# Kernel tuning notes

Hardware: AMD Instinct MI355X
Metric: run time of the kernel (lower is better)

The kernel has to match this reference:

```python
import jax, jax.numpy as jnp
import numpy as np

EPS_STAB = 1e-9   # numerical_stabilizer default
BN_EPS = 1e-5     # flax BatchNorm default epsilon


def setup_inputs() -> dict:
    key = jax.random.key(0)
    ks = jax.random.split(key, 5)
    B, N, C = 2, 4096, 512
    s = 1.0 / np.sqrt(C)
    d = {"inputs": jax.random.normal(ks[0], (B, N, C), jnp.float32)}
    # 1x1 convs == pointwise linear maps [C_in, C_out] + bias
    for i, w in enumerate(["Wq", "Wk", "Wv", "Wo"]):
        d[w] = jax.random.normal(ks[1 + i], (C, C), jnp.float32) * s
    for b in ["bq", "bk", "bv", "bo"]:
        d[b] = jnp.zeros((C,), jnp.float32)
    # BatchNorm (inference: use_running_average=True since train=False)
    d["bn_scale"] = jnp.ones((C,), jnp.float32)
    d["bn_bias"] = jnp.zeros((C,), jnp.float32)
    d["bn_mean"] = jnp.zeros((C,), jnp.float32)
    d["bn_var"] = jnp.ones((C,), jnp.float32)
    return d


def reference(inputs, Wq, bq, Wk, bk, Wv, bv, Wo, bo,
              bn_scale, bn_bias, bn_mean, bn_var):
    # QKV via 1x1 conv == dense projection. [B, N, C]
    q = inputs @ Wq + bq
    k = inputs @ Wk + bk
    v = inputs @ Wv + bv
    # scores [B, M, N]; softmax over last axis (N)
    att = jax.nn.softmax(jnp.einsum('bmc,bnc->bmn', q, k), axis=-1)
    # non-standard renorm: divide by column sums (axis=1 == M axis)
    att = att / (EPS_STAB + jnp.sum(att, axis=1, keepdims=True))
    # faithful to einsum '...MN,...NC->...NC': sum attention over M, scale v
    out = v * jnp.sum(att, axis=1)[..., None]
    # output 1x1 conv
    out = out @ Wo + bo
    # BatchNorm with running stats (feature axis -1)
    out = (out - bn_mean) * jax.lax.rsqrt(bn_var + BN_EPS) * bn_scale + bn_bias
    return jax.nn.relu(out) + inputs
```

## Files before the change

### kernel.cpp

```cpp
#include <hip/hip_runtime.h>
#include <hip/hip_bf16.h>

typedef unsigned short u16;
typedef unsigned int u32;
typedef __attribute__((ext_vector_type(8))) short short8;
typedef __attribute__((ext_vector_type(4))) float f32x4;
typedef __attribute__((ext_vector_type(4))) unsigned int u32x4;

__device__ __forceinline__ u16 f2bf(float f) {
    union { float f; unsigned u; } v; v.f = f;
    unsigned r = v.u + 0x7fffu + ((v.u >> 16) & 1u);
    return (u16)(r >> 16);
}

__device__ __forceinline__ float fexp2(float x) {
#if __has_builtin(__builtin_amdgcn_exp2f)
    return __builtin_amdgcn_exp2f(x);
#else
    return __expf(x * 0.6931471805599453f);
#endif
}

template <int CTRL>
__device__ __forceinline__ float fdpp(float x) {
    int xi = __builtin_bit_cast(int, x);
    int r = __builtin_amdgcn_update_dpp(0, xi, CTRL, 0xF, 0xF, true);
    return __builtin_bit_cast(float, r);
}
__device__ __forceinline__ float dpp_max16(float m) {
    m = fmaxf(m, fdpp<0xB1>(m));
    m = fmaxf(m, fdpp<0x4E>(m));
    m = fmaxf(m, fdpp<0x141>(m));
    m = fmaxf(m, fdpp<0x140>(m));
    return m;
}
__device__ __forceinline__ float dpp_sum16(float s) {
    s += fdpp<0xB1>(s);
    s += fdpp<0x4E>(s);
    s += fdpp<0x141>(s);
    s += fdpp<0x140>(s);
    return s;
}

#if __has_builtin(__builtin_amdgcn_cvt_pk_fp8_f32) && \
    __has_builtin(__builtin_amdgcn_cvt_f32_fp8)
#define FP8_HW 1
#else
#define FP8_HW 0
#endif

#if !FP8_HW
__device__ __forceinline__ u32 sw_fp8(float x) {
    union { float f; u32 u; } v; v.f = x;
    int E = (int)(v.u >> 23) - 127;
    if (x < 0.001953125f) return 0;
    if (E < -6) return (u32)(x * 512.0f + 0.5f);
    u32 m = v.u & 0x7fffffu;
    u32 r = (m + 0x80000u) >> 20;
    u32 bits = ((u32)(E + 7) << 3) + r;
    return bits > 0x7eu ? 0x7eu : bits;
}
__device__ __forceinline__ float sw_fp8d(u32 b) {
    u32 e = (b >> 3) & 15u, m = b & 7u;
    if (e == 0) return (float)m * 0.001953125f;
    union { u32 u; float f; } v; v.u = ((e + 120u) << 23) | (m << 20);
    return v.f;
}
#endif

__device__ __forceinline__ u32 fp8x4_pack(float p0, float p1, float p2, float p3) {
#if FP8_HW
    u32 v = (u32)__builtin_amdgcn_cvt_pk_fp8_f32(p0, p1, 0, false);
    v = (u32)__builtin_amdgcn_cvt_pk_fp8_f32(p2, p3, (int)v, true);
    return v;
#else
    return sw_fp8(p0) | (sw_fp8(p1) << 8) | (sw_fp8(p2) << 16) | (sw_fp8(p3) << 24);
#endif
}

#if FP8_HW
#define FP8_DEC(v, s) __builtin_amdgcn_cvt_f32_fp8((int)(v), (s))
#else
#define FP8_DEC(v, s) sw_fp8d(((v) >> ((s) * 8)) & 0xffu)
#endif

__device__ __forceinline__ void async_cp16(const u16* g, u16* l) {
    __builtin_amdgcn_global_load_lds(
        (const __attribute__((address_space(1))) void*)g,
        (__attribute__((address_space(3))) void*)l, 16, 0, 0);
}

__device__ __forceinline__ short8 mfma_ld(const u16* base, int off) {
    return *(const short8*)&base[off];
}

__device__ __forceinline__ void stage_half_A(const u16* __restrict__ Q,
                                             u16* dst, int kn, int half,
                                             int wid, int srow, int scol) {
#pragma unroll
    for (int c = 0; c < 2; c++) {
        int win = (wid >> 2) * 16 + half * 8 + (wid & 3) * 2 + c;
        async_cp16(Q + (size_t)(win * 8 + srow) * 512 + kn + scol,
                   dst + win * 512);
    }
}
__device__ __forceinline__ void stage_half_B(const u16* __restrict__ K,
                                             u16* dst, int kn, int half,
                                             int wid, int srow, int scol) {
#pragma unroll
    for (int c = 0; c < 2; c++) {
        int win = (wid >> 1) * 8 + half * 4 + (wid & 1) * 2 + c;
        async_cp16(K + (size_t)(win * 8 + srow) * 512 + kn + scol,
                   dst + win * 512);
    }
}

__device__ __forceinline__ void core256(const u16* __restrict__ A,
                                        const u16* __restrict__ B,
                                        u16* As0, u16* As1,
                                        u16* Bs0, u16* Bs1,
                                        f32x4 acc[8][4], int tid) {
    int lane = tid & 63, wid = tid >> 6;
    int quad = lane >> 4, l15 = lane & 15;
    int wm = wid >> 2, wn = wid & 3;
    int Gw = lane ^ ((lane >> 3) & 7);
    int srow = Gw >> 3, scol = (Gw & 7) * 8;
    int rl = l15 & 7, winl = l15 >> 3;
    int Pr[2];
#pragma unroll
    for (int h = 0; h < 2; h++)
        Pr[h] = (rl * 8 + ((quad + h * 4) ^ rl)) * 8;

    stage_half_A(A, As0, 0, 0, wid, srow, scol);
    stage_half_B(B, Bs0, 0, 0, wid, srow, scol);
    stage_half_B(B, Bs0, 0, 1, wid, srow, scol);
    stage_half_A(A, As0, 0, 1, wid, srow, scol);
    asm volatile("s_waitcnt vmcnt(0)" ::: "memory");
    __builtin_amdgcn_s_barrier();
    asm volatile("" ::: "memory");

    for (int kt = 0; kt < 8; ++kt) {
        const u16* Ac = (kt & 1) ? As1 : As0;
        const u16* Bc = (kt & 1) ? Bs1 : Bs0;
        u16* An = (kt & 1) ? As0 : As1;
        u16* Bn = (kt & 1) ? Bs0 : Bs1;
        int kn = (kt + 1) * 64;
        bool pf = (kt < 7);
        short8 af[4][2], bf0[2][2], bf1[2][2];
#pragma unroll
        for (int ph = 0; ph < 4; ++ph) {
            const int ih = ph >> 1;
            const int jh = (ph ^ (ph >> 1)) & 1;
            if (ph == 0) {
#pragma unroll
                for (int h = 0; h < 2; h++)
#pragma unroll
                    for (int ii = 0; ii < 4; ii++)
                        af[ii][h] = mfma_ld(
                            Ac, (wm * 16 + ii * 2 + winl) * 512 + Pr[h]);
#pragma unroll
                for (int h = 0; h < 2; h++)
#pragma unroll
                    for (int jj = 0; jj < 2; jj++)
                        bf0[jj][h] = mfma_ld(
                            Bc, (wn * 8 + jj * 2 + winl) * 512 + Pr[h]);
            } else if (ph == 1) {
#pragma unroll
                for (int h = 0; h < 2; h++)
#pragma unroll
                    for (int jj = 0; jj < 2; jj++)
                        bf1[jj][h] = mfma_ld(
                            Bc, (wn * 8 + 4 + jj * 2 + winl) * 512 + Pr[h]);
            } else if (ph == 2) {
#pragma unroll
                for (int h = 0; h < 2; h++)
#pragma unroll
                    for (int ii = 0; ii < 4; ii++)
                        af[ii][h] = mfma_ld(
                            Ac, (wm * 16 + 8 + ii * 2 + winl) * 512 + Pr[h]);
            }
            if (pf) {
                if (ph == 0) {
                    stage_half_A(A, An, kn, 0, wid, srow, scol);
                    stage_half_B(B, Bn, kn, 0, wid, srow, scol);
                } else if (ph == 1) {
                    stage_half_B(B, Bn, kn, 1, wid, srow, scol);
                } else if (ph == 2) {
                    stage_half_A(A, An, kn, 1, wid, srow, scol);
                }
            }
            if (ph == 1) {
                if (pf) asm volatile("s_waitcnt vmcnt(6)" ::: "memory");
                else    asm volatile("s_waitcnt vmcnt(0)" ::: "memory");
            }
            if (ph == 3) asm volatile("s_waitcnt vmcnt(2)" ::: "memory");
            asm volatile("" ::: "memory");
            __builtin_amdgcn_s_barrier();
            asm volatile("s_waitcnt lgkmcnt(0)" ::: "memory");
            __builtin_amdgcn_s_setprio(1);
            if (jh == 0) {
#pragma unroll
                for (int h = 0; h < 2; h++)
#pragma unroll
                    for (int ii = 0; ii < 4; ii++)
#pragma unroll
                        for (int jj = 0; jj < 2; jj++)
                            acc[ih * 4 + ii][jj] =
                                __builtin_amdgcn_mfma_f32_16x16x32_bf16(
                                    af[ii][h], bf0[jj][h],
                                    acc[ih * 4 + ii][jj], 0, 0, 0);
            } else {
#pragma unroll
                for (int h = 0; h < 2; h++)
#pragma unroll
                    for (int ii = 0; ii < 4; ii++)
#pragma unroll
                        for (int jj = 0; jj < 2; jj++)
                            acc[ih * 4 + ii][2 + jj] =
                                __builtin_amdgcn_mfma_f32_16x16x32_bf16(
                                    af[ii][h], bf1[jj][h],
                                    acc[ih * 4 + ii][2 + jj], 0, 0, 0);
            }
            __builtin_amdgcn_s_setprio(0);
            asm volatile("" ::: "memory");
            __builtin_amdgcn_s_barrier();
            asm volatile("" ::: "memory");
        }
    }
}

__device__ __forceinline__ void gemm512_r64(const u16* __restrict__ A,
                                            const u16* __restrict__ B,
                                            u16* As, u16* Bs,
                                            f32x4 acc[2][4], int tid) {
    const int lane = tid & 63, w = tid >> 6;
    const int quad = lane >> 4, l15 = lane & 15;
    const int wm = tid >> 7, wn = (tid >> 6) & 1;
    const int Gw = lane ^ ((lane >> 3) & 7);
    const int srow = Gw >> 3;
    const int scol = (Gw & 7) * 8;
    const int rl = l15 & 7;
    const int winl = l15 >> 3;
    int Pr[2];
#pragma unroll
    for (int h = 0; h < 2; h++)
        Pr[h] = (rl * 8 + ((quad + h * 4) ^ rl)) * 8;
    const int winA0 = (wm * 32) >> 3, winB0 = (wn * 64) >> 3;
    for (int k0 = 0; k0 < 512; k0 += 64) {
        __syncthreads();
#pragma unroll
        for (int t = 0; t < 2; t++) {
            int win = w * 2 + t;
            async_cp16(A + (size_t)(win * 8 + srow) * 512 + k0 + scol,
                       As + win * 512);
        }
#pragma unroll
        for (int t = 0; t < 4; t++) {
            int win = w * 4 + t;
            async_cp16(B + (size_t)(win * 8 + srow) * 512 + k0 + scol,
                       Bs + win * 512);
        }
        __syncthreads();
#pragma unroll
        for (int h = 0; h < 2; h++) {
            short8 af[2], bfr[4];
#pragma unroll
            for (int i = 0; i < 2; i++)
                af[i] = mfma_ld(As, (winA0 + i * 2 + winl) * 512 + Pr[h]);
#pragma unroll
            for (int j = 0; j < 4; j++)
                bfr[j] = mfma_ld(Bs, (winB0 + j * 2 + winl) * 512 + Pr[h]);
#pragma unroll
            for (int i = 0; i < 2; i++)
#pragma unroll
                for (int j = 0; j < 4; j++)
                    acc[i][j] = __builtin_amdgcn_mfma_f32_16x16x32_bf16(
                        af[i], bfr[j], acc[i][j], 0, 0, 0);
        }
    }
}

__global__ void prep(const float* __restrict__ X, const float* __restrict__ W0,
                     const float* __restrict__ W1, const float* __restrict__ W2,
                     const float* __restrict__ W3, u16* __restrict__ Xb,
                     u16* __restrict__ T0, u16* __restrict__ T1,
                     u16* __restrict__ T2, u16* __restrict__ T3,
                     float* __restrict__ Sg) {
    __shared__ float tile[32][33];
    int id = blockIdx.x, tid = threadIdx.x;
    if (id == 5120) {
        float4 z = {0.f, 0.f, 0.f, 0.f};
#pragma unroll
        for (int t = 0; t < 8; t++) ((float4*)Sg)[tid + t * 256] = z;
        return;
    }
    if (id < 4096) {
        int idx = (id * 256 + tid) * 4;
        float4 v = *(const float4*)&X[idx];
        ushort4 o;
        o.x = f2bf(v.x); o.y = f2bf(v.y); o.z = f2bf(v.z); o.w = f2bf(v.w);
        *(ushort4*)&Xb[idx] = o;
        return;
    }
    int t = id - 4096;
    int z = t >> 8, rem = t & 255;
    int bo_ = (rem & 15) * 32, bi = (rem >> 4) * 32;
    const float* src; u16* dst;
    switch (z) {
        case 0: src = W0; dst = T0; break;
        case 1: src = W1; dst = T1; break;
        case 2: src = W2; dst = T2; break;
        default: src = W3; dst = T3; break;
    }
    int tx = tid & 31, ty = tid >> 5;
#pragma unroll
    for (int s = 0; s < 4; s++) {
        int i = bi + ty + s * 8;
        tile[ty + s * 8][tx] = src[i * 512 + bo_ + tx];
    }
    __syncthreads();
#pragma unroll
    for (int s = 0; s < 4; s++) {
        int o = bo_ + ty + s * 8;
        dst[o * 512 + bi + tx] = f2bf(tile[tx][ty + s * 8]);
    }
}

__global__ __launch_bounds__(512, 2) void gemm_qkv(
    const u16* __restrict__ Xb, const u16* __restrict__ Wall,
    const float* __restrict__ bq, const float* __restrict__ bk,
    const float* __restrict__ bv, u16* __restrict__ Qall) {
    __shared__ __align__(16) u16 As[2][16384];
    __shared__ __align__(16) u16 Bs[2][16384];
    int tid = threadIdx.x;
    int m0 = blockIdx.x * 256, n0 = blockIdx.y * 256, z = blockIdx.z;
    const u16* A = Xb + (size_t)m0 * 512;
    const u16* B = Wall + (size_t)z * 262144 + (size_t)n0 * 512;
    f32x4 acc[8][4];
#pragma unroll
    for (int i = 0; i < 8; i++)
#pragma unroll
        for (int j = 0; j < 4; j++) acc[i][j] = (f32x4){0.f, 0.f, 0.f, 0.f};
    core256(A, B, &As[0][0], &As[1][0], &Bs[0][0], &Bs[1][0], acc, tid);

    const float* bias = (z == 0) ? bq : (z == 1) ? bk : bv;
    const float qs = (z == 0) ? 1.44269504088896340736f : 1.0f;
    u16* C = Qall + (size_t)z * 4194304;
    int lane = tid & 63, wid = tid >> 6;
    int quad = lane >> 4, l15 = lane & 15;
    int wm = wid >> 2, wn = wid & 3;
#pragma unroll
    for (int j = 0; j < 4; j++) {
        int n = n0 + wn * 64 + j * 16 + l15;
        float bvv = bias[n];
#pragma unroll
        for (int i = 0; i < 8; i++)
#pragma unroll
            for (int rg = 0; rg < 4; rg++) {
                int m = m0 + wm * 128 + i * 16 + quad * 4 + rg;
                C[(size_t)m * 512 + n] = f2bf((acc[i][j][rg] + bvv) * qs);
            }
    }
}

__global__ __launch_bounds__(512, 2) void attn_pass1p(
    const u16* __restrict__ Qb, const u16* __restrict__ Kb,
    float2* __restrict__ statsP, u32* __restrict__ Pbuf) {
    __shared__ __align__(16) u16 As[2][16384];
    __shared__ __align__(16) u16 Bs[2][16384];
    int tid = threadIdx.x;
    int mblk = blockIdx.x, nblk = blockIdx.y, b = blockIdx.z;
    const u16* Q = Qb + ((size_t)(b * 4096 + mblk * 256)) * 512;
    const u16* K = Kb + ((size_t)(b * 4096 + nblk * 256)) * 512;
    int lane = tid & 63, wid = tid >> 6;
    int quad = lane >> 4, l15 = lane & 15;
    int wm = wid >> 2, wn = wid & 3;

    f32x4 acc[8][4];
#pragma unroll
    for (int i = 0; i < 8; i++)
#pragma unroll
        for (int j = 0; j < 4; j++) acc[i][j] = (f32x4){0.f, 0.f, 0.f, 0.f};
    core256(Q, K, &As[0][0], &As[1][0], &Bs[0][0], &Bs[1][0], acc, tid);

    u32* Pt = Pbuf + ((size_t)((b * 16 + mblk) * 16 + nblk)) * 16384;
    int ch = nblk * 4 + wn;
    float2* Sp = statsP + ((size_t)(b * 64 + ch)) * 4096;
    int mbase = mblk * 256 + wm * 128;
#pragma unroll
    for (int i = 0; i < 8; i++) {
        u32x4 pk;
#pragma unroll
        for (int rg = 0; rg < 4; rg++) {
            float v0 = acc[i][0][rg], v1 = acc[i][1][rg];
            float v2 = acc[i][2][rg], v3 = acc[i][3][rg];
            float Mt = fmaxf(fmaxf(v0, v1), fmaxf(v2, v3));
            Mt = dpp_max16(Mt);
            float e8 = Mt - 8.0f;
            float p0 = fexp2(v0 - e8), p1 = fexp2(v1 - e8);
            float p2 = fexp2(v2 - e8), p3 = fexp2(v3 - e8);
            pk[rg] = fp8x4_pack(p0, p1, p2, p3);
            float L = dpp_sum16(p0 + p1 + p2 + p3);
            if (l15 == 0)
                Sp[mbase + i * 16 + quad * 4 + rg] =
                    make_float2(Mt, L * 0.00390625f);
        }
        *(u32x4*)&Pt[i * 2048 + tid * 4] = pk;
    }
}

__global__ void reduce_stats2(const float2* __restrict__ statsP,
                              float* __restrict__ cstat) {
    int t = blockIdx.x * 256 + threadIdx.x;
    int b = t >> 12, m = t & 4095;
    const float2* sp = statsP + (size_t)b * 64 * 4096 + m;
    float M = -INFINITY;
#pragma unroll 4
    for (int ch = 0; ch < 64; ch++) M = fmaxf(M, sp[(size_t)ch * 4096].x);
    float Z = 0.f;
#pragma unroll 4
    for (int ch = 0; ch < 64; ch++) {
        float2 p = sp[(size_t)ch * 4096];
        Z += p.y * fexp2(p.x - M);
    }
    cstat[t] = M + __log2f(Z);
}

__global__ __launch_bounds__(512) void colsum(
    const u32* __restrict__ Pbuf, const float2* __restrict__ statsP,
    const float* __restrict__ cstat, float* __restrict__ Sg) {
    int tid = threadIdx.x, lane = tid & 63, wid = tid >> 6;
    int quad = lane >> 4, l15 = lane & 15;
    int wm = wid >> 2, wn = wid & 3;
    int nblk = blockIdx.x, mgrp = blockIdx.y, b = blockIdx.z;
    int ch = nblk * 4 + wn;
    const float2* Sp = statsP + ((size_t)(b * 64 + ch)) * 4096;
    const float* Cp = cstat + (size_t)b * 4096;
    float cp[4] = {0.f, 0.f, 0.f, 0.f};
    for (int mb = 0; mb < 2; mb++) {
        int mblk = mgrp * 2 + mb;
        const u32* Pt =
            Pbuf + ((size_t)((b * 16 + mblk) * 16 + nblk)) * 16384;
#pragma unroll
        for (int i = 0; i < 8; i++) {
            int r0 = mblk * 256 + wm * 128 + i * 16 + quad * 4;
            float4 s01 = *(const float4*)&Sp[r0];
            float4 s23 = *(const float4*)&Sp[r0 + 2];
            float4 cv = *(const float4*)&Cp[r0];
            float fv[4] = {fexp2(s01.x - 8.0f - cv.x),
                           fexp2(s01.z - 8.0f - cv.y),
                           fexp2(s23.x - 8.0f - cv.z),
                           fexp2(s23.z - 8.0f - cv.w)};
            float fm = fmaxf(fmaxf(fv[0], fv[1]), fmaxf(fv[2], fv[3]));
            if (fm > 3.469446951953614e-18f) {
                u32x4 e4 = *(const u32x4*)&Pt[i * 2048 + tid * 4];
#pragma unroll
                for (int rg = 0; rg < 4; rg++) {
                    u32 e = e4[rg];
                    cp[0] += FP8_DEC(e, 0) * fv[rg];
                    cp[1] += FP8_DEC(e, 1) * fv[rg];
                    cp[2] += FP8_DEC(e, 2) * fv[rg];
                    cp[3] += FP8_DEC(e, 3) * fv[rg];
                }
            }
        }
    }
#pragma unroll
    for (int j = 0; j < 4; j++) {
        float s = cp[j];
        s += __shfl_xor(s, 16);
        s += __shfl_xor(s, 32);
        if (lane < 16)
            atomicAdd(&Sg[b * 4096 + nblk * 256 + wn * 64 + j * 16 + l15], s);
    }
}

__global__ __launch_bounds__(256) void gemm_final(
    const u16* __restrict__ A, const u16* __restrict__ Bt,
    const float* __restrict__ Sg, const float* __restrict__ bo,
    const float* __restrict__ g, const float* __restrict__ bb,
    const float* __restrict__ mean, const float* __restrict__ var,
    const float* __restrict__ X, float* __restrict__ out) {
    __shared__ __align__(16) u16 As[4096];
    __shared__ __align__(16) u16 Bs[8192];
    int tid = threadIdx.x;
    int m0 = blockIdx.x * 64, n0 = blockIdx.y * 128;
    f32x4 acc[2][4];
#pragma unroll
    for (int i = 0; i < 2; i++)
#pragma unroll
        for (int j = 0; j < 4; j++) acc[i][j] = (f32x4){0.f, 0.f, 0.f, 0.f};
    gemm512_r64(A + (size_t)m0 * 512, Bt + (size_t)n0 * 512, As, Bs, acc, tid);
    int lane = tid & 63, quad = lane >> 4, l15 = lane & 15;
    int wm = tid >> 7, wn = (tid >> 6) & 1;
    float sc[2][4];
#pragma unroll
    for (int i = 0; i < 2; i++) {
        float4 s = *(const float4*)&Sg[m0 + wm * 32 + i * 16 + quad * 4];
        float v[4] = {s.x, s.y, s.z, s.w};
#pragma unroll
        for (int rg = 0; rg < 4; rg++) sc[i][rg] = v[rg] / (1e-9f + v[rg]);
    }
#pragma unroll
    for (int j = 0; j < 4; j++) {
        int n = n0 + wn * 64 + j * 16 + l15;
        float aj = rsqrtf(var[n] + 1e-5f) * g[n];
        float cj = bb[n] - mean[n] * aj;
        float bj = bo[n];
#pragma unroll
        for (int i = 0; i < 2; i++)
#pragma unroll
            for (int rg = 0; rg < 4; rg++) {
                int m = m0 + wm * 32 + i * 16 + quad * 4 + rg;
                float x = acc[i][j][rg] * sc[i][rg] + bj;
                float y = x * aj + cj;
                out[(size_t)m * 512 + n] = fmaxf(y, 0.f) + X[(size_t)m * 512 + n];
            }
    }
}

extern "C" void kernel_launch(void* const* d_in, const int* in_sizes, int n_in,
                              void* d_out, int out_size, void* d_ws, size_t ws_size,
                              hipStream_t stream) {
    const float* X  = (const float*)d_in[0];
    const float* Wq = (const float*)d_in[1];
    const float* Wk = (const float*)d_in[2];
    const float* Wv = (const float*)d_in[3];
    const float* Wo = (const float*)d_in[4];
    const float* bq = (const float*)d_in[5];
    const float* bk = (const float*)d_in[6];
    const float* bv = (const float*)d_in[7];
    const float* bo = (const float*)d_in[8];
    const float* g    = (const float*)d_in[9];
    const float* bb   = (const float*)d_in[10];
    const float* mean = (const float*)d_in[11];
    const float* var  = (const float*)d_in[12];
    float* out = (float*)d_out;

    char* ws = (char*)d_ws;
    u16* Xb  = (u16*)(ws + 0);
    u16* Wqt = (u16*)(ws + 8388608);
    u16* Wot = (u16*)(ws + 9961472);
    u16* Qb  = (u16*)(ws + 10485760);
    u16* Kb  = (u16*)(ws + 18874368);
    u16* Vb  = (u16*)(ws + 27262976);
    float2* statsP = (float2*)(ws + 35651584);
    float* Sg      = (float*)(ws + 39845888);
    float* cstat   = (float*)(ws + 39878656);
    u32* Pbuf      = (u32*)(ws + 39911424);

    prep<<<5121, 256, 0, stream>>>(X, Wq, Wk, Wv, Wo, Xb, Wqt, Wqt + 262144,
                                   Wqt + 524288, Wot, Sg);
    gemm_qkv<<<dim3(32, 2, 3), 512, 0, stream>>>(Xb, Wqt, bq, bk, bv, Qb);
    attn_pass1p<<<dim3(16, 16, 2), 512, 0, stream>>>(Qb, Kb, statsP, Pbuf);
    reduce_stats2<<<32, 256, 0, stream>>>(statsP, cstat);
    colsum<<<dim3(16, 8, 2), 512, 0, stream>>>(Pbuf, statsP, cstat, Sg);
    gemm_final<<<dim3(128, 4), 256, 0, stream>>>(Vb, Wot, Sg, bo, g, bb, mean, var,
                                                 X, out);
}
```

Baseline: 200.6 us.

## Software-pipeline LDS fragment loads across MFMA phases in core256 GEMM

Restructures the 256-tile GEMM main loop into fully unrolled per-k-tile steps in which shared-memory fragment loads for the next phase (and for the next k-tile's first A/B fragments) are issued before the current phase's MFMAs. The lgkmcnt(0) wait before each MFMA block is removed and the MFMA quadrant order is reordered so that loaded fragments are reused. The goal is to hide LDS read latency behind matrix math. In exchange it holds more fragment registers live, which may raise register pressure, and it adds more barriers per k-tile.

```diff
diff --git a/kernel.cpp b/kernel.cpp
--- a/kernel.cpp
+++ b/kernel.cpp
@@ -113,6 +113,96 @@
         async_cp16(K + (size_t)(win * 8 + srow) * 512 + kn + scol,
                    dst + win * 512);
     }
+}
+
+__device__ __forceinline__ void ld_a(const u16* S, short8 af[4][2], int row0,
+                                     int winl, const int* Pr) {
+#pragma unroll
+    for (int h = 0; h < 2; h++)
+#pragma unroll
+        for (int ii = 0; ii < 4; ii++)
+            af[ii][h] = mfma_ld(S, (row0 + ii * 2 + winl) * 512 + Pr[h]);
+}
+__device__ __forceinline__ void ld_b(const u16* S, short8 bf[2][2], int row0,
+                                     int winl, const int* Pr) {
+#pragma unroll
+    for (int h = 0; h < 2; h++)
+#pragma unroll
+        for (int jj = 0; jj < 2; jj++)
+            bf[jj][h] = mfma_ld(S, (row0 + jj * 2 + winl) * 512 + Pr[h]);
+}
+__device__ __forceinline__ void mfma8(f32x4 acc[8][4], int i0, int j0,
+                                      const short8 af[4][2],
+                                      const short8 bf[2][2]) {
+#pragma unroll
+    for (int h = 0; h < 2; h++)
+#pragma unroll
+        for (int ii = 0; ii < 4; ii++)
+#pragma unroll
+            for (int jj = 0; jj < 2; jj++)
+                acc[i0 + ii][j0 + jj] = __builtin_amdgcn_mfma_f32_16x16x32_bf16(
+                    af[ii][h], bf[jj][h], acc[i0 + ii][j0 + jj], 0, 0, 0);
+}
+
+template <int KT>
+__device__ __forceinline__ void kt_step(
+    const u16* __restrict__ A, const u16* __restrict__ B,
+    const u16* Ac, const u16* Bc, u16* An, u16* Bn,
+    short8 afL[4][2], short8 afH[4][2], short8 bf0c[2][2], short8 bf0n[2][2],
+    short8 bf1[2][2], f32x4 acc[8][4], int wid, int srow, int scol, int wm,
+    int wn, int winl, const int* Pr) {
+    const int kn = (KT + 1) * 64;
+    constexpr bool pf = (KT < 7);
+    if (pf) {
+        stage_half_A(A, An, kn, 0, wid, srow, scol);
+        stage_half_B(B, Bn, kn, 0, wid, srow, scol);
+    }
+    __builtin_amdgcn_s_barrier();
+    asm volatile("" ::: "memory");
+    ld_b(Bc, bf1, wn * 8 + 4, winl, Pr);
+    __builtin_amdgcn_s_setprio(1);
+    mfma8(acc, 0, 0, afL, bf0c);
+    __builtin_amdgcn_s_setprio(0);
+    asm volatile("" ::: "memory");
+    __builtin_amdgcn_s_barrier();
+    asm volatile("" ::: "memory");
+    if (pf) {
+        stage_half_B(B, Bn, kn, 1, wid, srow, scol);
+        asm volatile("s_waitcnt vmcnt(6)" ::: "memory");
+    } else {
+        asm volatile("s_waitcnt vmcnt(0)" ::: "memory");
+    }
+    __builtin_amdgcn_s_barrier();
+    asm volatile("" ::: "memory");
+    ld_a(Ac, afH, wm * 16 + 8, winl, Pr);
+    __builtin_amdgcn_s_setprio(1);
+    mfma8(acc, 0, 2, afL, bf1);
+    __builtin_amdgcn_s_setprio(0);
+    asm volatile("" ::: "memory");
+    __builtin_amdgcn_s_barrier();
+    asm volatile("" ::: "memory");
+    if (pf) stage_half_A(A, An, kn, 1, wid, srow, scol);
+    __builtin_amdgcn_s_barrier();
+    asm volatile("" ::: "memory");
+    __builtin_amdgcn_s_setprio(1);
+    mfma8(acc, 4, 2, afH, bf1);
+    __builtin_amdgcn_s_setprio(0);
+    asm volatile("" ::: "memory");
+    __builtin_amdgcn_s_barrier();
+    asm volatile("" ::: "memory");
+    asm volatile("s_waitcnt vmcnt(2)" ::: "memory");
+    __builtin_amdgcn_s_barrier();
+    asm volatile("" ::: "memory");
+    if (pf) {
+        ld_a(An, afL, wm * 16, winl, Pr);
+        ld_b(Bn, bf0n, wn * 8, winl, Pr);
+    }
+    __builtin_amdgcn_s_setprio(1);
+    mfma8(acc, 4, 0, afH, bf0c);
+    __builtin_amdgcn_s_setprio(0);
+    asm volatile("" ::: "memory");
+    __builtin_amdgcn_s_barrier();
+    asm volatile("" ::: "memory");
 }
 
 __device__ __forceinline__ void core256(const u16* __restrict__ A,
@@ -131,6 +221,8 @@
     for (int h = 0; h < 2; h++)
         Pr[h] = (rl * 8 + ((quad + h * 4) ^ rl)) * 8;
 
+    short8 afL[4][2], afH[4][2], bf0a[2][2], bf0b[2][2], bf1[2][2];
+
     stage_half_A(A, As0, 0, 0, wid, srow, scol);
     stage_half_B(B, Bs0, 0, 0, wid, srow, scol);
     stage_half_B(B, Bs0, 0, 1, wid, srow, scol);
@@ -138,95 +230,25 @@
     asm volatile("s_waitcnt vmcnt(0)" ::: "memory");
     __builtin_amdgcn_s_barrier();
     asm volatile("" ::: "memory");
-
-    for (int kt = 0; kt < 8; ++kt) {
-        const u16* Ac = (kt & 1) ? As1 : As0;
-        const u16* Bc = (kt & 1) ? Bs1 : Bs0;
-        u16* An = (kt & 1) ? As0 : As1;
-        u16* Bn = (kt & 1) ? Bs0 : Bs1;
-        int kn = (kt + 1) * 64;
-        bool pf = (kt < 7);
-        short8 af[4][2], bf0[2][2], bf1[2][2];
-#pragma unroll
-        for (int ph = 0; ph < 4; ++ph) {
-            const int ih = ph >> 1;
-            const int jh = (ph ^ (ph >> 1)) & 1;
-            if (ph == 0) {
-#pragma unroll
-                for (int h = 0; h < 2; h++)
-#pragma unroll
-                    for (int ii = 0; ii < 4; ii++)
-                        af[ii][h] = mfma_ld(
-                            Ac, (wm * 16 + ii * 2 + winl) * 512 + Pr[h]);
-#pragma unroll
-                for (int h = 0; h < 2; h++)
-#pragma unroll
-                    for (int jj = 0; jj < 2; jj++)
-                        bf0[jj][h] = mfma_ld(
-                            Bc, (wn * 8 + jj * 2 + winl) * 512 + Pr[h]);
-            } else if (ph == 1) {
-#pragma unroll
-                for (int h = 0; h < 2; h++)
-#pragma unroll
-                    for (int jj = 0; jj < 2; jj++)
-                        bf1[jj][h] = mfma_ld(
-                            Bc, (wn * 8 + 4 + jj * 2 + winl) * 512 + Pr[h]);
-            } else if (ph == 2) {
-#pragma unroll
-                for (int h = 0; h < 2; h++)
-#pragma unroll
-                    for (int ii = 0; ii < 4; ii++)
-                        af[ii][h] = mfma_ld(
-                            Ac, (wm * 16 + 8 + ii * 2 + winl) * 512 + Pr[h]);
-            }
-            if (pf) {
-                if (ph == 0) {
-                    stage_half_A(A, An, kn, 0, wid, srow, scol);
-                    stage_half_B(B, Bn, kn, 0, wid, srow, scol);
-                } else if (ph == 1) {
-                    stage_half_B(B, Bn, kn, 1, wid, srow, scol);
-                } else if (ph == 2) {
-                    stage_half_A(A, An, kn, 1, wid, srow, scol);
-                }
-            }
-            if (ph == 1) {
-                if (pf) asm volatile("s_waitcnt vmcnt(6)" ::: "memory");
-                else    asm volatile("s_waitcnt vmcnt(0)" ::: "memory");
-            }
-            if (ph == 3) asm volatile("s_waitcnt vmcnt(2)" ::: "memory");
-            asm volatile("" ::: "memory");
-            __builtin_amdgcn_s_barrier();
-            asm volatile("s_waitcnt lgkmcnt(0)" ::: "memory");
-            __builtin_amdgcn_s_setprio(1);
-            if (jh == 0) {
-#pragma unroll
-                for (int h = 0; h < 2; h++)
-#pragma unroll
-                    for (int ii = 0; ii < 4; ii++)
-#pragma unroll
-                        for (int jj = 0; jj < 2; jj++)
-                            acc[ih * 4 + ii][jj] =
-                                __builtin_amdgcn_mfma_f32_16x16x32_bf16(
-                                    af[ii][h], bf0[jj][h],
-                                    acc[ih * 4 + ii][jj], 0, 0, 0);
-            } else {
-#pragma unroll
-                for (int h = 0; h < 2; h++)
-#pragma unroll
-                    for (int ii = 0; ii < 4; ii++)
-#pragma unroll
-                        for (int jj = 0; jj < 2; jj++)
-                            acc[ih * 4 + ii][2 + jj] =
-                                __builtin_amdgcn_mfma_f32_16x16x32_bf16(
-                                    af[ii][h], bf1[jj][h],
-                                    acc[ih * 4 + ii][2 + jj], 0, 0, 0);
-            }
-            __builtin_amdgcn_s_setprio(0);
-            asm volatile("" ::: "memory");
-            __builtin_amdgcn_s_barrier();
-            asm volatile("" ::: "memory");
-        }
-    }
+    ld_a(As0, afL, wm * 16, winl, Pr);
+    ld_b(Bs0, bf0a, wn * 8, winl, Pr);
+
+    kt_step<0>(A, B, As0, Bs0, As1, Bs1, afL, afH, bf0a, bf0b, bf1, acc,
+               wid, srow, scol, wm, wn, winl, Pr);
+    kt_step<1>(A, B, As1, Bs1, As0, Bs0, afL, afH, bf0b, bf0a, bf1, acc,
+               wid, srow, scol, wm, wn, winl, Pr);
+    kt_step<2>(A, B, As0, Bs0, As1, Bs1, afL, afH, bf0a, bf0b, bf1, acc,
+               wid, srow, scol, wm, wn, winl, Pr);
+    kt_step<3>(A, B, As1, Bs1, As0, Bs0, afL, afH, bf0b, bf0a, bf1, acc,
+               wid, srow, scol, wm, wn, winl, Pr);
+    kt_step<4>(A, B, As0, Bs0, As1, Bs1, afL, afH, bf0a, bf0b, bf1, acc,
+               wid, srow, scol, wm, wn, winl, Pr);
+    kt_step<5>(A, B, As1, Bs1, As0, Bs0, afL, afH, bf0b, bf0a, bf1, acc,
+               wid, srow, scol, wm, wn, winl, Pr);
+    kt_step<6>(A, B, As0, Bs0, As1, Bs1, afL, afH, bf0a, bf0b, bf1, acc,
+               wid, srow, scol, wm, wn, winl, Pr);
+    kt_step<7>(A, B, As1, Bs1, As0, Bs0, afL, afH, bf0b, bf0a, bf1, acc,
+               wid, srow, scol, wm, wn, winl, Pr);
 }
 
 __device__ __forceinline__ void gemm512_r64(const u16* __restrict__ A,
```

Measured after the change: 199.8 us. Within noise of the previous version (-0.4%).

## Fuse all pipeline stages into one cooperative persistent kernel with grid syncs

Applied to the files above, without the earlier changes.

Replaces the six separate kernel launches with a single cooperative kernel of 256 blocks that runs prep, QKV GEMM, score/softmax pass, stats reduction plus column sum, and the final GEMM in phases separated by grid.sync(). The aim is to remove launch gaps and inter-kernel tails. The stats reduction is now recomputed redundantly in each colsum block instead of a separate kernel. The cost is reduced parallelism in some phases: only 192 of 256 blocks work in the QKV GEMM, the attention pass needs two rounds per block, and grid barriers are added. The old multi-kernel path is kept as a fallback if the cooperative launch fails.

```diff
diff --git a/kernel.cpp b/kernel.cpp
--- a/kernel.cpp
+++ b/kernel.cpp
@@ -1,5 +1,8 @@
 #include <hip/hip_runtime.h>
 #include <hip/hip_bf16.h>
+#include <hip/hip_cooperative_groups.h>
+
+namespace cg = cooperative_groups;
 
 typedef unsigned short u16;
 typedef unsigned int u32;
@@ -280,6 +283,249 @@
     }
 }
 
+__global__ __launch_bounds__(512, 2) void mega(
+    const float* __restrict__ X, const float* __restrict__ W0,
+    const float* __restrict__ W1, const float* __restrict__ W2,
+    const float* __restrict__ W3, const float* __restrict__ bq,
+    const float* __restrict__ bk, const float* __restrict__ bv,
+    const float* __restrict__ bo, const float* __restrict__ g,
+    const float* __restrict__ bb, const float* __restrict__ mean,
+    const float* __restrict__ var, u16* __restrict__ Xb,
+    u16* __restrict__ Wqt, u16* __restrict__ Qall,
+    float2* __restrict__ statsP, float* __restrict__ Sg,
+    u32* __restrict__ Pbuf, float* __restrict__ out) {
+    __shared__ __align__(16) u16 arena[65536];
+    int bid = blockIdx.x, tid = threadIdx.x;
+    cg::grid_group grid = cg::this_grid();
+
+    {
+#pragma unroll
+        for (int r = 0; r < 8; r++) {
+            int idx4 = bid * 512 + tid + r * 131072;
+            float4 v = ((const float4*)X)[idx4];
+            ushort4 o;
+            o.x = f2bf(v.x); o.y = f2bf(v.y); o.z = f2bf(v.z); o.w = f2bf(v.w);
+            ((ushort4*)Xb)[idx4] = o;
+        }
+        if (bid == 0) {
+            float4 z4 = {0.f, 0.f, 0.f, 0.f};
+#pragma unroll
+            for (int r = 0; r < 4; r++) ((float4*)Sg)[tid + r * 512] = z4;
+        }
+        int h = tid >> 8, tl = tid & 255;
+        int tx = tl & 31, ty = tl >> 5;
+        float* fa = (float*)arena;
+        float (*tile)[33] = (float(*)[33])(fa + h * 1056);
+        for (int u = bid * 2 + h; u < 1024; u += 512) {
+            int z = u >> 8, rem = u & 255;
+            int bo_ = (rem & 15) * 32, bi = (rem >> 4) * 32;
+            const float* src; u16* dst;
+            switch (z) {
+                case 0: src = W0; dst = Wqt; break;
+                case 1: src = W1; dst = Wqt + 262144; break;
+                case 2: src = W2; dst = Wqt + 524288; break;
+                default: src = W3; dst = Wqt + 786432; break;
+            }
+#pragma unroll
+            for (int s = 0; s < 4; s++)
+                tile[ty + s * 8][tx] =
+                    src[(size_t)(bi + ty + s * 8) * 512 + bo_ + tx];
+            __syncthreads();
+#pragma unroll
+            for (int s = 0; s < 4; s++)
+                dst[(size_t)(bo_ + ty + s * 8) * 512 + bi + tx] =
+                    f2bf(tile[tx][ty + s * 8]);
+            __syncthreads();
+        }
+    }
+    grid.sync();
+
+    if (bid < 192) {
+        int z = bid >> 6, q = bid & 63;
+        int m0 = (q >> 1) * 256, n0 = (q & 1) * 256;
+        const u16* A = Xb + (size_t)m0 * 512;
+        const u16* B = Wqt + (size_t)z * 262144 + (size_t)n0 * 512;
+        f32x4 acc[8][4];
+#pragma unroll
+        for (int i = 0; i < 8; i++)
+#pragma unroll
+            for (int j = 0; j < 4; j++) acc[i][j] = (f32x4){0.f, 0.f, 0.f, 0.f};
+        core256(A, B, arena, arena + 16384, arena + 32768, arena + 49152,
+                acc, tid);
+        const float* bias = (z == 0) ? bq : (z == 1) ? bk : bv;
+        const float qs = (z == 0) ? 1.44269504088896340736f : 1.0f;
+        u16* C = Qall + (size_t)z * 4194304;
+        int lane = tid & 63, wid = tid >> 6;
+        int quad = lane >> 4, l15 = lane & 15;
+        int wm = wid >> 2, wn = wid & 3;
+#pragma unroll
+        for (int j = 0; j < 4; j++) {
+            int n = n0 + wn * 64 + j * 16 + l15;
+            float bvv = bias[n];
+#pragma unroll
+            for (int i = 0; i < 8; i++)
+#pragma unroll
+                for (int rg = 0; rg < 4; rg++) {
+                    int m = m0 + wm * 128 + i * 16 + quad * 4 + rg;
+                    C[(size_t)m * 512 + n] = f2bf((acc[i][j][rg] + bvv) * qs);
+                }
+        }
+    }
+    grid.sync();
+
+    for (int rr = 0; rr < 2; rr++) {
+        int t = bid + rr * 256;
+        int mblk = t & 15, nblk = (t >> 4) & 15, b = t >> 8;
+        const u16* Q = Qall + ((size_t)(b * 4096 + mblk * 256)) * 512;
+        const u16* K = Qall + 4194304 + ((size_t)(b * 4096 + nblk * 256)) * 512;
+        f32x4 acc[8][4];
+#pragma unroll
+        for (int i = 0; i < 8; i++)
+#pragma unroll
+            for (int j = 0; j < 4; j++) acc[i][j] = (f32x4){0.f, 0.f, 0.f, 0.f};
+        core256(Q, K, arena, arena + 16384, arena + 32768, arena + 49152,
+                acc, tid);
+        int lane = tid & 63, wid = tid >> 6;
+        int quad = lane >> 4, l15 = lane & 15;
+        int wm = wid >> 2, wn = wid & 3;
+        u32* Pt = Pbuf + ((size_t)((b * 16 + mblk) * 16 + nblk)) * 16384;
+        int ch = nblk * 4 + wn;
+        float2* Sp = statsP + ((size_t)(b * 64 + ch)) * 4096;
+        int mbase = mblk * 256 + wm * 128;
+#pragma unroll
+        for (int i = 0; i < 8; i++) {
+            u32x4 pk;
+#pragma unroll
+            for (int rg = 0; rg < 4; rg++) {
+                float v0 = acc[i][0][rg], v1 = acc[i][1][rg];
+                float v2 = acc[i][2][rg], v3 = acc[i][3][rg];
+                float Mt = fmaxf(fmaxf(v0, v1), fmaxf(v2, v3));
+                Mt = dpp_max16(Mt);
+                float e8 = Mt - 8.0f;
+                float p0 = fexp2(v0 - e8), p1 = fexp2(v1 - e8);
+                float p2 = fexp2(v2 - e8), p3 = fexp2(v3 - e8);
+                pk[rg] = fp8x4_pack(p0, p1, p2, p3);
+                float L = dpp_sum16(p0 + p1 + p2 + p3);
+                if (l15 == 0)
+                    Sp[mbase + i * 16 + quad * 4 + rg] =
+                        make_float2(Mt, L * 0.00390625f);
+            }
+            *(u32x4*)&Pt[i * 2048 + tid * 4] = pk;
+        }
+    }
+    grid.sync();
+
+    {
+        int nblk = bid & 15, mgrp = (bid >> 4) & 7, b = bid >> 7;
+        float* cs = (float*)arena;
+        {
+            int m = mgrp * 512 + tid;
+            const float2* sp = statsP + (size_t)b * 64 * 4096 + m;
+            float M = -INFINITY;
+#pragma unroll 4
+            for (int ch = 0; ch < 64; ch++)
+                M = fmaxf(M, sp[(size_t)ch * 4096].x);
+            float Z = 0.f;
+#pragma unroll 4
+            for (int ch = 0; ch < 64; ch++) {
+                float2 p = sp[(size_t)ch * 4096];
+                Z += p.y * fexp2(p.x - M);
+            }
+            cs[tid] = M + __log2f(Z);
+        }
+        __syncthreads();
+        int lane = tid & 63, wid = tid >> 6;
+        int quad = lane >> 4, l15 = lane & 15;
+        int wm = wid >> 2, wn = wid & 3;
+        int ch = nblk * 4 + wn;
+        const float2* Sp = statsP + ((size_t)(b * 64 + ch)) * 4096;
+        float cp[4] = {0.f, 0.f, 0.f, 0.f};
+        for (int mb = 0; mb < 2; mb++) {
+            int mblk = mgrp * 2 + mb;
+            const u32* Pt =
+                Pbuf + ((size_t)((b * 16 + mblk) * 16 + nblk)) * 16384;
+#pragma unroll
+            for (int i = 0; i < 8; i++) {
+                int r0 = mblk * 256 + wm * 128 + i * 16 + quad * 4;
+                float4 s01 = *(const float4*)&Sp[r0];
+                float4 s23 = *(const float4*)&Sp[r0 + 2];
+                int rl0 = mb * 256 + wm * 128 + i * 16 + quad * 4;
+                float4 cv = *(const float4*)&cs[rl0];
+                float fv[4] = {fexp2(s01.x - 8.0f - cv.x),
+                               fexp2(s01.z - 8.0f - cv.y),
+                               fexp2(s23.x - 8.0f - cv.z),
+                               fexp2(s23.z - 8.0f - cv.w)};
+                float fm = fmaxf(fmaxf(fv[0], fv[1]), fmaxf(fv[2], fv[3]));
+                if (fm > 3.469446951953614e-18f) {
+                    u32x4 e4 = *(const u32x4*)&Pt[i * 2048 + tid * 4];
+#pragma unroll
+                    for (int rg = 0; rg < 4; rg++) {
+                        u32 e = e4[rg];
+                        cp[0] += FP8_DEC(e, 0) * fv[rg];
+                        cp[1] += FP8_DEC(e, 1) * fv[rg];
+                        cp[2] += FP8_DEC(e, 2) * fv[rg];
+                        cp[3] += FP8_DEC(e, 3) * fv[rg];
+                    }
+                }
+            }
+        }
+#pragma unroll
+        for (int j = 0; j < 4; j++) {
+            float s = cp[j];
+            s += __shfl_xor(s, 16);
+            s += __shfl_xor(s, 32);
+            if (lane < 16)
+                atomicAdd(&Sg[b * 4096 + nblk * 256 + wn * 64 + j * 16 + l15],
+                          s);
+        }
+    }
+    grid.sync();
+
+    {
+        int h = tid >> 8, tl = tid & 255;
+        int ft = bid * 2 + h;
+        int m0 = (ft >> 2) * 64, n0 = (ft & 3) * 128;
+        const u16* Vb = Qall + 8388608;
+        const u16* Bt = Wqt + 786432;
+        u16* As_h = arena + h * 16384;
+        u16* Bs_h = arena + 32768 + h * 16384;
+        f32x4 acc[2][4];
+#pragma unroll
+        for (int i = 0; i < 2; i++)
+#pragma unroll
+            for (int j = 0; j < 4; j++) acc[i][j] = (f32x4){0.f, 0.f, 0.f, 0.f};
+        gemm512_r64(Vb + (size_t)m0 * 512, Bt + (size_t)n0 * 512, As_h, Bs_h,
+                    acc, tl);
+        int lane = tl & 63, quad = lane >> 4, l15 = lane & 15;
+        int wm = tl >> 7, wn = (tl >> 6) & 1;
+        float sc[2][4];
+#pragma unroll
+        for (int i = 0; i < 2; i++) {
+            float4 s = *(const float4*)&Sg[m0 + wm * 32 + i * 16 + quad * 4];
+            float v[4] = {s.x, s.y, s.z, s.w};
+#pragma unroll
+            for (int rg = 0; rg < 4; rg++) sc[i][rg] = v[rg] / (1e-9f + v[rg]);
+        }
+#pragma unroll
+        for (int j = 0; j < 4; j++) {
+            int n = n0 + wn * 64 + j * 16 + l15;
+            float aj = rsqrtf(var[n] + 1e-5f) * g[n];
+            float cj = bb[n] - mean[n] * aj;
+            float bj = bo[n];
+#pragma unroll
+            for (int i = 0; i < 2; i++)
+#pragma unroll
+                for (int rg = 0; rg < 4; rg++) {
+                    int m = m0 + wm * 32 + i * 16 + quad * 4 + rg;
+                    float x = acc[i][j][rg] * sc[i][rg] + bj;
+                    float y = x * aj + cj;
+                    out[(size_t)m * 512 + n] =
+                        fmaxf(y, 0.f) + X[(size_t)m * 512 + n];
+                }
+        }
+    }
+}
+
 __global__ void prep(const float* __restrict__ X, const float* __restrict__ W0,
                      const float* __restrict__ W1, const float* __restrict__ W2,
                      const float* __restrict__ W3, u16* __restrict__ Xb,
@@ -342,7 +588,6 @@
 #pragma unroll
         for (int j = 0; j < 4; j++) acc[i][j] = (f32x4){0.f, 0.f, 0.f, 0.f};
     core256(A, B, &As[0][0], &As[1][0], &Bs[0][0], &Bs[1][0], acc, tid);
-
     const float* bias = (z == 0) ? bq : (z == 1) ? bk : bv;
     const float qs = (z == 0) ? 1.44269504088896340736f : 1.0f;
     u16* C = Qall + (size_t)z * 4194304;
@@ -375,14 +620,12 @@
     int lane = tid & 63, wid = tid >> 6;
     int quad = lane >> 4, l15 = lane & 15;
     int wm = wid >> 2, wn = wid & 3;
-
     f32x4 acc[8][4];
 #pragma unroll
     for (int i = 0; i < 8; i++)
 #pragma unroll
         for (int j = 0; j < 4; j++) acc[i][j] = (f32x4){0.f, 0.f, 0.f, 0.f};
     core256(Q, K, &As[0][0], &As[1][0], &Bs[0][0], &Bs[1][0], acc, tid);
-
     u32* Pt = Pbuf + ((size_t)((b * 16 + mblk) * 16 + nblk)) * 16384;
     int ch = nblk * 4 + wn;
     float2* Sp = statsP + ((size_t)(b * 64 + ch)) * 4096;
@@ -549,12 +792,18 @@
     float* cstat   = (float*)(ws + 39878656);
     u32* Pbuf      = (u32*)(ws + 39911424);
 
-    prep<<<5121, 256, 0, stream>>>(X, Wq, Wk, Wv, Wo, Xb, Wqt, Wqt + 262144,
-                                   Wqt + 524288, Wot, Sg);
-    gemm_qkv<<<dim3(32, 2, 3), 512, 0, stream>>>(Xb, Wqt, bq, bk, bv, Qb);
-    attn_pass1p<<<dim3(16, 16, 2), 512, 0, stream>>>(Qb, Kb, statsP, Pbuf);
-    reduce_stats2<<<32, 256, 0, stream>>>(statsP, cstat);
-    colsum<<<dim3(16, 8, 2), 512, 0, stream>>>(Pbuf, statsP, cstat, Sg);
-    gemm_final<<<dim3(128, 4), 256, 0, stream>>>(Vb, Wot, Sg, bo, g, bb, mean, var,
-                                                 X, out);
-}
+    void* args[] = {&X,  &Wq, &Wk, &Wv, &Wo, &bq, &bk,  &bv, &bo, &g,
+                    &bb, &mean, &var, &Xb, &Wqt, &Qb, &statsP, &Sg, &Pbuf, &out};
+    hipError_t e = hipLaunchCooperativeKernel((const void*)mega, dim3(256),
+                                              dim3(512), args, 0, stream);
+    if (e != hipSuccess) {
+        prep<<<5121, 256, 0, stream>>>(X, Wq, Wk, Wv, Wo, Xb, Wqt,
+                                       Wqt + 262144, Wqt + 524288, Wot, Sg);
+        gemm_qkv<<<dim3(32, 2, 3), 512, 0, stream>>>(Xb, Wqt, bq, bk, bv, Qb);
+        attn_pass1p<<<dim3(16, 16, 2), 512, 0, stream>>>(Qb, Kb, statsP, Pbuf);
+        reduce_stats2<<<32, 256, 0, stream>>>(statsP, cstat);
+        colsum<<<dim3(16, 8, 2), 512, 0, stream>>>(Pbuf, statsP, cstat, Sg);
+        gemm_final<<<dim3(128, 4), 256, 0, stream>>>(Vb, Wot, Sg, bo, g, bb,
+                                                     mean, var, X, out);
+    }
+}
```

Measured after the change: 363.9 us. 1.81x slower.
